# Optimization experiments

Measured on AMD Instinct MI355X. Metric: run time of the kernel, lower is better.

The kernel has to match this reference:

```python
import jax, jax.numpy as jnp
import numpy as np

N_NODES = 10000
N_EDGES = 160000
F_DIM = 64
H = 4


def setup_inputs() -> dict:
    key = jax.random.key(0)
    ks = jax.random.split(key, 10)
    s = 1.0 / np.sqrt(F_DIM)  # xavier-ish scale
    return {
        "x": jax.random.normal(ks[0], (N_NODES, F_DIM), jnp.float32),
        "edge_index": jax.random.randint(ks[1], (2, N_EDGES), 0, N_NODES),
        "edge_vec": jax.random.normal(ks[2], (N_EDGES, 3), jnp.float32),
        "edge_len": jax.random.uniform(ks[3], (N_EDGES,), jnp.float32, 0.1, 5.0),
        "w_proj_W": jax.random.normal(ks[4], (H, F_DIM, F_DIM), jnp.float32) * s,
        "radial_W": jax.random.normal(ks[5], (H, F_DIM, F_DIM), jnp.float32) * s,
        "tangential_W": jax.random.normal(ks[6], (H, F_DIM, F_DIM), jnp.float32) * s,
        "radial_score": jax.random.normal(ks[7], (H, F_DIM), jnp.float32) * s,
        "tangential_score": jax.random.normal(ks[8], (H, F_DIM), jnp.float32) * s,
        "radial_distance_log_scale": jnp.zeros((), jnp.float32),
        "radial_temp_bias": jnp.zeros((H,), jnp.float32),
        "radial_temp_weight": jnp.zeros((H,), jnp.float32),
        "w_out_W": jax.random.normal(ks[9], (F_DIM, F_DIM), jnp.float32) * s,
    }


def _segment_softmax(logits, receiver, num_nodes):
    # logits: [E, H]; softmax over all edges sharing the same receiver.
    # Equivalent to the original's degree-bucketed per-group softmax.
    m = jax.ops.segment_max(logits, receiver, num_segments=num_nodes)  # [N, H]
    a = jnp.exp(logits - m[receiver])
    d = jax.ops.segment_sum(a, receiver, num_segments=num_nodes)       # [N, H]
    return a / d[receiver]


def reference(x, edge_index, edge_vec, edge_len, w_proj_W, radial_W, tangential_W,
              radial_score, tangential_score, radial_distance_log_scale,
              radial_temp_bias, radial_temp_weight, w_out_W):
    sender, receiver = edge_index[0], edge_index[1]
    n = x.shape[0]

    # Per-head bias-free linear projections (o3.Linear on scalar irreps).
    energy = jnp.einsum('nf,hfg->hng', x, w_proj_W)       # [H, N, F]
    radial = jnp.einsum('nf,hfg->hng', x, radial_W)       # [H, N, F]
    tang = jnp.einsum('nf,hfg->hng', x, tangential_W)     # [H, N, F]

    e_d = energy[:, sender] - energy[:, receiver]                       # [H, E, F]
    r_d = jnp.transpose(radial[:, sender] - radial[:, receiver], (1, 0, 2))  # [E, H, F]
    t_d = jnp.transpose(tang[:, sender] - tang[:, receiver], (1, 0, 2))      # [E, H, F]

    scale = jax.nn.softplus(radial_distance_log_scale)
    r_log = jnp.einsum('hef,hf->eh', e_d, radial_score) - scale * edge_len[:, None]  # [E, H]
    temp = jax.nn.softplus(radial_temp_bias[None, :] + radial_temp_weight[None, :] * edge_len[:, None])
    r_log = r_log / (temp + 0.0001)
    t_log = jnp.einsum('hef,hf->eh', e_d, tangential_score)                          # [E, H]

    r_alpha = _segment_softmax(r_log, receiver, n)  # [E, H]
    t_alpha = _segment_softmax(t_log, receiver, n)  # [E, H]

    r_msg = jax.ops.segment_sum(r_alpha[:, :, None] * r_d, receiver, num_segments=n)  # [N, H, F]
    t_msg = jax.ops.segment_sum(t_alpha[:, :, None] * t_d, receiver, num_segments=n)  # [N, H, F]

    out = jnp.nan_to_num((r_msg + t_msg).mean(axis=1))  # mean over heads -> [N, F]
    return x + out @ w_out_W
```

## Files before the change

### kernel.cpp

```cpp
#include <hip/hip_runtime.h>
#include <math.h>

#define N_NODES 10000
#define N_EDGES 160000
#define CAP 64

typedef short bf16x8 __attribute__((ext_vector_type(8)));
typedef float f32x4 __attribute__((ext_vector_type(4)));

__device__ __forceinline__ float bf2f(unsigned short u) {
    return __uint_as_float(((unsigned int)u) << 16);
}
__device__ __forceinline__ unsigned short f2bf(float f) {
    unsigned int x = __float_as_uint(f);
    unsigned int r = (x + 0x7fffu + ((x >> 16) & 1u)) >> 16;
    return (unsigned short)r;
}
__device__ __forceinline__ float softplus_f(float x) {
    return fmaxf(x, 0.f) + log1pf(expf(-fabsf(x)));
}

#define NB_PROJ 628
#define NB_SCORE 40
#define NB_BUCKET 625

__global__ void __launch_bounds__(256) k_prep(const float* __restrict__ x,
                                              const float* __restrict__ wrad,
                                              const float* __restrict__ wtan,
                                              const float* __restrict__ wproj,
                                              const float* __restrict__ rsc,
                                              const float* __restrict__ tsc,
                                              const int* __restrict__ ei,
                                              const float* __restrict__ el,
                                              unsigned short* __restrict__ radb,
                                              unsigned short* __restrict__ tanb,
                                              float* __restrict__ rs,
                                              float* __restrict__ ts,
                                              int* __restrict__ cur,
                                              int2* __restrict__ sbuf) {
    __shared__ __align__(16) char smem[2 * 64 * 72 * 2];
    int b = blockIdx.x;
    int t = threadIdx.x;

    if (b < NB_PROJ) {
        unsigned short* wt0 = (unsigned short*)smem;
        unsigned short* wt1 = wt0 + 64 * 72;
        int h = b & 3;
        int nb = (b >> 2) * 64;
        const float* wr = wrad + h * 4096;
        const float* wtp = wtan + h * 4096;
        for (int i = 0; i < 16; ++i) {
            int e = t + 256 * i;
            int f = e >> 6, g = e & 63;
            wt0[g * 72 + f] = f2bf(wr[e]);
            wt1[g * 72 + f] = f2bf(wtp[e]);
        }
        __syncthreads();

        int wid = t >> 6, lane = t & 63;
        int q = lane >> 4, l16 = lane & 15;
        int node = nb + wid * 16 + l16;
        int nrow = min(node, N_NODES - 1);

        bf16x8 bfr[2];
#pragma unroll
        for (int kc = 0; kc < 2; ++kc) {
            const float* xp = x + nrow * 64 + kc * 32 + q * 8;
            float4 v0 = ((const float4*)xp)[0];
            float4 v1 = ((const float4*)xp)[1];
            bf16x8 bv;
            bv[0] = (short)f2bf(v0.x); bv[1] = (short)f2bf(v0.y);
            bv[2] = (short)f2bf(v0.z); bv[3] = (short)f2bf(v0.w);
            bv[4] = (short)f2bf(v1.x); bv[5] = (short)f2bf(v1.y);
            bv[6] = (short)f2bf(v1.z); bv[7] = (short)f2bf(v1.w);
            bfr[kc] = bv;
        }
#pragma unroll
        for (int gt = 0; gt < 4; ++gt) {
            f32x4 accr = {0.f, 0.f, 0.f, 0.f};
            f32x4 acct = {0.f, 0.f, 0.f, 0.f};
            int arow = gt * 16 + l16;
#pragma unroll
            for (int kc = 0; kc < 2; ++kc) {
                bf16x8 ar = *(const bf16x8*)&wt0[arow * 72 + kc * 32 + q * 8];
                bf16x8 at = *(const bf16x8*)&wt1[arow * 72 + kc * 32 + q * 8];
                accr = __builtin_amdgcn_mfma_f32_16x16x32_bf16(ar, bfr[kc], accr, 0, 0, 0);
                acct = __builtin_amdgcn_mfma_f32_16x16x32_bf16(at, bfr[kc], acct, 0, 0, 0);
            }
            if (node < N_NODES) {
                int g = gt * 16 + q * 4;
                ushort4 rv = make_ushort4(f2bf(accr[0]), f2bf(accr[1]),
                                          f2bf(accr[2]), f2bf(accr[3]));
                ushort4 tv = make_ushort4(f2bf(acct[0]), f2bf(acct[1]),
                                          f2bf(acct[2]), f2bf(acct[3]));
                *(ushort4*)(radb + node * 256 + h * 64 + g) = rv;
                *(ushort4*)(tanb + node * 256 + h * 64 + g) = tv;
            }
        }
    } else if (b < NB_PROJ + NB_SCORE) {
        float* vrl = (float*)smem;
        float* vtl = vrl + 256;
        {
            int h = t >> 6, f = t & 63;
            const float* wrow = wproj + h * 4096 + f * 64;
            const float* rsp = rsc + h * 64;
            const float* tsp = tsc + h * 64;
            float ar = 0.f, at = 0.f;
            for (int g = 0; g < 64; ++g) {
                float w = wrow[g];
                ar += w * rsp[g];
                at += w * tsp[g];
            }
            vrl[t] = ar;
            vtl[t] = at;
        }
        __syncthreads();
        int n = (b - NB_PROJ) * 256 + t;
        if (n >= N_NODES) return;
        const float4* xr = (const float4*)(x + n * 64);
        float accr[4] = {0.f, 0.f, 0.f, 0.f};
        float acct[4] = {0.f, 0.f, 0.f, 0.f};
        for (int i = 0; i < 16; ++i) {
            float4 xv = xr[i];
#pragma unroll
            for (int h = 0; h < 4; ++h) {
                float4 a = ((const float4*)vrl)[h * 16 + i];
                accr[h] += xv.x * a.x + xv.y * a.y + xv.z * a.z + xv.w * a.w;
                float4 bb = ((const float4*)vtl)[h * 16 + i];
                acct[h] += xv.x * bb.x + xv.y * bb.y + xv.z * bb.z + xv.w * bb.w;
            }
        }
        ((float4*)rs)[n] = make_float4(accr[0], accr[1], accr[2], accr[3]);
        ((float4*)ts)[n] = make_float4(acct[0], acct[1], acct[2], acct[3]);
    } else {
        int e = (b - NB_PROJ - NB_SCORE) * 256 + t;
        if (e >= N_EDGES) return;
        int s = ei[e];
        int r = ei[N_EDGES + e];
        float len = el[e];
        int pos = atomicAdd(&cur[r], 1);
        if (pos < CAP) sbuf[r * CAP + pos] = make_int2(s, __float_as_int(len));
    }
}

__global__ void __launch_bounds__(256) k_node(const int* __restrict__ cur,
                                              const int2* __restrict__ sbuf,
                                              const float* __restrict__ rs,
                                              const float* __restrict__ ts,
                                              const unsigned short* __restrict__ radb,
                                              const unsigned short* __restrict__ tanb,
                                              const float* __restrict__ rdls,
                                              const float* __restrict__ tb,
                                              const float* __restrict__ tw,
                                              const float* __restrict__ x,
                                              const float* __restrict__ wout,
                                              float* __restrict__ out) {
    __shared__ float wl[4096];
    __shared__ float alds[4][CAP][8];
    __shared__ int   slds[4][CAP];
    __shared__ float prelds[4][64];
    int t = threadIdx.x;
    for (int i = 0; i < 16; ++i) wl[t + 256 * i] = wout[t + 256 * i];

    int wid = t >> 6, lane = t & 63;
    int n = blockIdx.x * 4 + wid;
    int deg = min(cur[n], CAP);

    float4 rsr = ((const float4*)rs)[n];
    float4 tsr = ((const float4*)ts)[n];
    float scale = softplus_f(rdls[0]);
    float tb0 = tb[0], tb1 = tb[1], tb2 = tb[2], tb3 = tb[3];
    float tw0 = tw[0], tw1 = tw[1], tw2 = tw[2], tw3 = tw[3];

    const float NEG = -3.402823466e38f;
    float rl0 = NEG, rl1 = NEG, rl2 = NEG, rl3 = NEG;
    float tl0 = NEG, tl1 = NEG, tl2 = NEG, tl3 = NEG;
    int s_e = 0;
    if (lane < deg) {
        int2 sl = sbuf[n * CAP + lane];
        s_e = sl.x;
        float len = __int_as_float(sl.y);
        float4 rss = ((const float4*)rs)[s_e];
        float4 tss = ((const float4*)ts)[s_e];
        float sl0 = scale * len;
        float i0 = 1.f / (softplus_f(tb0 + tw0 * len) + 1e-4f);
        float i1 = 1.f / (softplus_f(tb1 + tw1 * len) + 1e-4f);
        float i2 = 1.f / (softplus_f(tb2 + tw2 * len) + 1e-4f);
        float i3 = 1.f / (softplus_f(tb3 + tw3 * len) + 1e-4f);
        rl0 = ((rss.x - rsr.x) - sl0) * i0;
        rl1 = ((rss.y - rsr.y) - sl0) * i1;
        rl2 = ((rss.z - rsr.z) - sl0) * i2;
        rl3 = ((rss.w - rsr.w) - sl0) * i3;
        tl0 = tss.x - tsr.x;
        tl1 = tss.y - tsr.y;
        tl2 = tss.z - tsr.z;
        tl3 = tss.w - tsr.w;
    }
    float mr0 = rl0, mr1 = rl1, mr2 = rl2, mr3 = rl3;
    float mt0 = tl0, mt1 = tl1, mt2 = tl2, mt3 = tl3;
#pragma unroll
    for (int d = 32; d >= 1; d >>= 1) {
        mr0 = fmaxf(mr0, __shfl_xor(mr0, d)); mr1 = fmaxf(mr1, __shfl_xor(mr1, d));
        mr2 = fmaxf(mr2, __shfl_xor(mr2, d)); mr3 = fmaxf(mr3, __shfl_xor(mr3, d));
        mt0 = fmaxf(mt0, __shfl_xor(mt0, d)); mt1 = fmaxf(mt1, __shfl_xor(mt1, d));
        mt2 = fmaxf(mt2, __shfl_xor(mt2, d)); mt3 = fmaxf(mt3, __shfl_xor(mt3, d));
    }
    float er0 = 0.f, er1 = 0.f, er2 = 0.f, er3 = 0.f;
    float et0 = 0.f, et1 = 0.f, et2 = 0.f, et3 = 0.f;
    if (lane < deg) {
        er0 = expf(rl0 - mr0); er1 = expf(rl1 - mr1);
        er2 = expf(rl2 - mr2); er3 = expf(rl3 - mr3);
        et0 = expf(tl0 - mt0); et1 = expf(tl1 - mt1);
        et2 = expf(tl2 - mt2); et3 = expf(tl3 - mt3);
    }
    float sr0 = er0, sr1 = er1, sr2 = er2, sr3 = er3;
    float st0 = et0, st1 = et1, st2 = et2, st3 = et3;
#pragma unroll
    for (int d = 32; d >= 1; d >>= 1) {
        sr0 += __shfl_xor(sr0, d); sr1 += __shfl_xor(sr1, d);
        sr2 += __shfl_xor(sr2, d); sr3 += __shfl_xor(sr3, d);
        st0 += __shfl_xor(st0, d); st1 += __shfl_xor(st1, d);
        st2 += __shfl_xor(st2, d); st3 += __shfl_xor(st3, d);
    }
    if (lane < deg) {
        float* ap = &alds[wid][lane][0];
        ((float4*)ap)[0] = make_float4(er0 / sr0, er1 / sr1, er2 / sr2, er3 / sr3);
        ((float4*)ap)[1] = make_float4(et0 / st0, et1 / st1, et2 / st2, et3 / st3);
        slds[wid][lane] = s_e;
    }

    int h = lane >> 4;
    int hb = h * 64 + ((lane & 15) << 2);
    float a0 = 0.f, a1 = 0.f, a2 = 0.f, a3 = 0.f;
    float b0 = 0.f, b1 = 0.f, b2 = 0.f, b3 = 0.f;
    int i = 0;
    for (; i + 2 <= deg; i += 2) {
        int s0 = slds[wid][i], s1 = slds[wid][i + 1];
        float ar0 = alds[wid][i][h],     at0 = alds[wid][i][4 + h];
        float ar1 = alds[wid][i + 1][h], at1 = alds[wid][i + 1][4 + h];
        ushort4 rv0 = *(const ushort4*)(radb + s0 * 256 + hb);
        ushort4 tv0 = *(const ushort4*)(tanb + s0 * 256 + hb);
        ushort4 rv1 = *(const ushort4*)(radb + s1 * 256 + hb);
        ushort4 tv1 = *(const ushort4*)(tanb + s1 * 256 + hb);
        a0 += ar0 * bf2f(rv0.x) + ar1 * bf2f(rv1.x);
        a1 += ar0 * bf2f(rv0.y) + ar1 * bf2f(rv1.y);
        a2 += ar0 * bf2f(rv0.z) + ar1 * bf2f(rv1.z);
        a3 += ar0 * bf2f(rv0.w) + ar1 * bf2f(rv1.w);
        b0 += at0 * bf2f(tv0.x) + at1 * bf2f(tv1.x);
        b1 += at0 * bf2f(tv0.y) + at1 * bf2f(tv1.y);
        b2 += at0 * bf2f(tv0.z) + at1 * bf2f(tv1.z);
        b3 += at0 * bf2f(tv0.w) + at1 * bf2f(tv1.w);
    }
    if (i < deg) {
        int s0 = slds[wid][i];
        float ar0 = alds[wid][i][h], at0 = alds[wid][i][4 + h];
        ushort4 rv0 = *(const ushort4*)(radb + s0 * 256 + hb);
        ushort4 tv0 = *(const ushort4*)(tanb + s0 * 256 + hb);
        a0 += ar0 * bf2f(rv0.x); a1 += ar0 * bf2f(rv0.y);
        a2 += ar0 * bf2f(rv0.z); a3 += ar0 * bf2f(rv0.w);
        b0 += at0 * bf2f(tv0.x); b1 += at0 * bf2f(tv0.y);
        b2 += at0 * bf2f(tv0.z); b3 += at0 * bf2f(tv0.w);
    }
    if (deg > 0) {
        ushort4 rv = *(const ushort4*)(radb + n * 256 + hb);
        ushort4 tv = *(const ushort4*)(tanb + n * 256 + hb);
        a0 -= bf2f(rv.x); a1 -= bf2f(rv.y); a2 -= bf2f(rv.z); a3 -= bf2f(rv.w);
        b0 -= bf2f(tv.x); b1 -= bf2f(tv.y); b2 -= bf2f(tv.z); b3 -= bf2f(tv.w);
    }
    float c0 = a0 + b0, c1 = a1 + b1, c2 = a2 + b2, c3 = a3 + b3;
    c0 += __shfl_xor(c0, 16); c0 += __shfl_xor(c0, 32);
    c1 += __shfl_xor(c1, 16); c1 += __shfl_xor(c1, 32);
    c2 += __shfl_xor(c2, 16); c2 += __shfl_xor(c2, 32);
    c3 += __shfl_xor(c3, 16); c3 += __shfl_xor(c3, 32);
    if (lane < 16) {
        ((float4*)&prelds[wid][0])[lane] =
            make_float4(c0 * 0.25f, c1 * 0.25f, c2 * 0.25f, c3 * 0.25f);
    }
    __syncthreads();

    float acc = 0.f;
    const float* pw = &prelds[wid][0];
#pragma unroll 4
    for (int gc = 0; gc < 16; ++gc) {
        float4 pv = ((const float4*)pw)[gc];
        acc += pv.x * wl[(4 * gc + 0) * 64 + lane];
        acc += pv.y * wl[(4 * gc + 1) * 64 + lane];
        acc += pv.z * wl[(4 * gc + 2) * 64 + lane];
        acc += pv.w * wl[(4 * gc + 3) * 64 + lane];
    }
    out[n * 64 + lane] = x[n * 64 + lane] + acc;
}

extern "C" void kernel_launch(void* const* d_in, const int* in_sizes, int n_in,
                              void* d_out, int out_size, void* d_ws, size_t ws_size,
                              hipStream_t stream) {
    const float* x     = (const float*)d_in[0];
    const int*   ei    = (const int*)d_in[1];
    const float* el    = (const float*)d_in[3];
    const float* wproj = (const float*)d_in[4];
    const float* wrad  = (const float*)d_in[5];
    const float* wtan  = (const float*)d_in[6];
    const float* rsc   = (const float*)d_in[7];
    const float* tsc   = (const float*)d_in[8];
    const float* rdls  = (const float*)d_in[9];
    const float* tb    = (const float*)d_in[10];
    const float* tw    = (const float*)d_in[11];
    const float* wout  = (const float*)d_in[12];
    float* out = (float*)d_out;

    char* w = (char*)d_ws;
    size_t o = 0;
    auto nxt = [&](size_t bytes) -> char* {
        char* p = w + o;
        o += (bytes + 255) & ~(size_t)255;
        return p;
    };
    unsigned short* radb = (unsigned short*)nxt((size_t)N_NODES * 256 * 2);
    unsigned short* tanb = (unsigned short*)nxt((size_t)N_NODES * 256 * 2);
    float* rs = (float*)nxt((size_t)N_NODES * 4 * 4);
    float* ts = (float*)nxt((size_t)N_NODES * 4 * 4);
    int*   cur = (int*)nxt((size_t)N_NODES * 4);
    int2*  sbuf = (int2*)nxt((size_t)N_NODES * CAP * 8);

    hipMemsetAsync(cur, 0, (size_t)N_NODES * 4, stream);

    k_prep<<<NB_PROJ + NB_SCORE + NB_BUCKET, 256, 0, stream>>>(
        x, wrad, wtan, wproj, rsc, tsc, ei, el, radb, tanb, rs, ts, cur, sbuf);
    k_node<<<2500, 256, 0, stream>>>(cur, sbuf, rs, ts, radb, tanb,
                                     rdls, tb, tw, x, wout, out);
}
```

Baseline: 132.9 us.

## Aggregate raw x per head then apply pre-multiplied projection·Wout via MFMA

The per-node radial and tangential projections are no longer precomputed. Each node instead accumulates attention-weighted raw sender x rows per head, and the receiver-term subtraction is handled by the same contraction. Combined weight matrices (per-head W·Wout, plus the negated sum for the self term, with the 1/4 head mean folded in) are built in the prep kernel. A 16-node block then does a 576-deep bf16 MFMA against them. This removes the 628 projection blocks and the bf16 radb/tanb gather traffic, but puts more FMA work into aggregation and a larger GEMM per block.

```diff
diff --git a/kernel.cpp b/kernel.cpp
--- a/kernel.cpp
+++ b/kernel.cpp
@@ -4,6 +4,11 @@
 #define N_NODES 10000
 #define N_EDGES 160000
 #define CAP 64
+
+#define NB_SCORE 40
+#define NB_BUCKET 625
+#define NB_WPP 9
+#define NB_D1 (NB_SCORE + NB_BUCKET + NB_WPP)
 
 typedef short bf16x8 __attribute__((ext_vector_type(8)));
 typedef float f32x4 __attribute__((ext_vector_type(4)));
@@ -20,86 +25,27 @@
     return fmaxf(x, 0.f) + log1pf(expf(-fabsf(x)));
 }
 
-#define NB_PROJ 628
-#define NB_SCORE 40
-#define NB_BUCKET 625
-
 __global__ void __launch_bounds__(256) k_prep(const float* __restrict__ x,
+                                              const float* __restrict__ wproj,
                                               const float* __restrict__ wrad,
                                               const float* __restrict__ wtan,
-                                              const float* __restrict__ wproj,
                                               const float* __restrict__ rsc,
                                               const float* __restrict__ tsc,
+                                              const float* __restrict__ wout,
                                               const int* __restrict__ ei,
                                               const float* __restrict__ el,
-                                              unsigned short* __restrict__ radb,
-                                              unsigned short* __restrict__ tanb,
                                               float* __restrict__ rs,
                                               float* __restrict__ ts,
                                               int* __restrict__ cur,
-                                              int2* __restrict__ sbuf) {
-    __shared__ __align__(16) char smem[2 * 64 * 72 * 2];
+                                              int2* __restrict__ sbuf,
+                                              unsigned short* __restrict__ wppT) {
+    __shared__ __align__(16) float smem[8192];
     int b = blockIdx.x;
     int t = threadIdx.x;
 
-    if (b < NB_PROJ) {
-        unsigned short* wt0 = (unsigned short*)smem;
-        unsigned short* wt1 = wt0 + 64 * 72;
-        int h = b & 3;
-        int nb = (b >> 2) * 64;
-        const float* wr = wrad + h * 4096;
-        const float* wtp = wtan + h * 4096;
-        for (int i = 0; i < 16; ++i) {
-            int e = t + 256 * i;
-            int f = e >> 6, g = e & 63;
-            wt0[g * 72 + f] = f2bf(wr[e]);
-            wt1[g * 72 + f] = f2bf(wtp[e]);
-        }
-        __syncthreads();
-
-        int wid = t >> 6, lane = t & 63;
-        int q = lane >> 4, l16 = lane & 15;
-        int node = nb + wid * 16 + l16;
-        int nrow = min(node, N_NODES - 1);
-
-        bf16x8 bfr[2];
-#pragma unroll
-        for (int kc = 0; kc < 2; ++kc) {
-            const float* xp = x + nrow * 64 + kc * 32 + q * 8;
-            float4 v0 = ((const float4*)xp)[0];
-            float4 v1 = ((const float4*)xp)[1];
-            bf16x8 bv;
-            bv[0] = (short)f2bf(v0.x); bv[1] = (short)f2bf(v0.y);
-            bv[2] = (short)f2bf(v0.z); bv[3] = (short)f2bf(v0.w);
-            bv[4] = (short)f2bf(v1.x); bv[5] = (short)f2bf(v1.y);
-            bv[6] = (short)f2bf(v1.z); bv[7] = (short)f2bf(v1.w);
-            bfr[kc] = bv;
-        }
-#pragma unroll
-        for (int gt = 0; gt < 4; ++gt) {
-            f32x4 accr = {0.f, 0.f, 0.f, 0.f};
-            f32x4 acct = {0.f, 0.f, 0.f, 0.f};
-            int arow = gt * 16 + l16;
-#pragma unroll
-            for (int kc = 0; kc < 2; ++kc) {
-                bf16x8 ar = *(const bf16x8*)&wt0[arow * 72 + kc * 32 + q * 8];
-                bf16x8 at = *(const bf16x8*)&wt1[arow * 72 + kc * 32 + q * 8];
-                accr = __builtin_amdgcn_mfma_f32_16x16x32_bf16(ar, bfr[kc], accr, 0, 0, 0);
-                acct = __builtin_amdgcn_mfma_f32_16x16x32_bf16(at, bfr[kc], acct, 0, 0, 0);
-            }
-            if (node < N_NODES) {
-                int g = gt * 16 + q * 4;
-                ushort4 rv = make_ushort4(f2bf(accr[0]), f2bf(accr[1]),
-                                          f2bf(accr[2]), f2bf(accr[3]));
-                ushort4 tv = make_ushort4(f2bf(acct[0]), f2bf(acct[1]),
-                                          f2bf(acct[2]), f2bf(acct[3]));
-                *(ushort4*)(radb + node * 256 + h * 64 + g) = rv;
-                *(ushort4*)(tanb + node * 256 + h * 64 + g) = tv;
-            }
-        }
-    } else if (b < NB_PROJ + NB_SCORE) {
-        float* vrl = (float*)smem;
-        float* vtl = vrl + 256;
+    if (b < NB_SCORE) {
+        float* vrl = smem;
+        float* vtl = smem + 256;
         {
             int h = t >> 6, f = t & 63;
             const float* wrow = wproj + h * 4096 + f * 64;
@@ -115,7 +61,7 @@
             vtl[t] = at;
         }
         __syncthreads();
-        int n = (b - NB_PROJ) * 256 + t;
+        int n = b * 256 + t;
         if (n >= N_NODES) return;
         const float4* xr = (const float4*)(x + n * 64);
         float accr[4] = {0.f, 0.f, 0.f, 0.f};
@@ -132,14 +78,40 @@
         }
         ((float4*)rs)[n] = make_float4(accr[0], accr[1], accr[2], accr[3]);
         ((float4*)ts)[n] = make_float4(acct[0], acct[1], acct[2], acct[3]);
-    } else {
-        int e = (b - NB_PROJ - NB_SCORE) * 256 + t;
+    } else if (b < NB_SCORE + NB_BUCKET) {
+        int e = (b - NB_SCORE) * 256 + t;
         if (e >= N_EDGES) return;
         int s = ei[e];
         int r = ei[N_EDGES + e];
         float len = el[e];
         int pos = atomicAdd(&cur[r], 1);
         if (pos < CAP) sbuf[r * CAP + pos] = make_int2(s, __float_as_int(len));
+    } else {
+        int k = b - NB_SCORE - NB_BUCKET;
+        float* wo = smem;
+        float* am = smem + 4096;
+        for (int i = 0; i < 16; ++i) wo[t + 256 * i] = wout[t + 256 * i];
+        if (k < 8) {
+            const float* M = (k < 4) ? (wrad + k * 4096) : (wtan + (k - 4) * 4096);
+            for (int i = 0; i < 16; ++i) am[t + 256 * i] = M[t + 256 * i];
+        } else {
+            for (int i = 0; i < 16; ++i) {
+                int e = t + 256 * i;
+                float s = 0.f;
+#pragma unroll
+                for (int h = 0; h < 4; ++h) s += wrad[h * 4096 + e] + wtan[h * 4096 + e];
+                am[e] = -s;
+            }
+        }
+        __syncthreads();
+        int c = t & 63;
+        int fg = t >> 6;
+        for (int j = 0; j < 16; ++j) {
+            int f = fg * 16 + j;
+            float acc = 0.f;
+            for (int g = 0; g < 64; ++g) acc += am[f * 64 + g] * wo[g * 64 + c];
+            wppT[c * 576 + k * 64 + f] = f2bf(acc * 0.25f);
+        }
     }
 }
 
@@ -147,148 +119,149 @@
                                               const int2* __restrict__ sbuf,
                                               const float* __restrict__ rs,
                                               const float* __restrict__ ts,
-                                              const unsigned short* __restrict__ radb,
-                                              const unsigned short* __restrict__ tanb,
                                               const float* __restrict__ rdls,
                                               const float* __restrict__ tb,
                                               const float* __restrict__ tw,
                                               const float* __restrict__ x,
-                                              const float* __restrict__ wout,
+                                              const unsigned short* __restrict__ wppT,
                                               float* __restrict__ out) {
-    __shared__ float wl[4096];
-    __shared__ float alds[4][CAP][8];
-    __shared__ int   slds[4][CAP];
-    __shared__ float prelds[4][64];
+    __shared__ __align__(16) unsigned short accL[16 * 584];
+    __shared__ __align__(16) float aldsb[4][CAP * 8];
+    __shared__ int sldsb[4][CAP];
     int t = threadIdx.x;
-    for (int i = 0; i < 16; ++i) wl[t + 256 * i] = wout[t + 256 * i];
-
     int wid = t >> 6, lane = t & 63;
-    int n = blockIdx.x * 4 + wid;
-    int deg = min(cur[n], CAP);
-
-    float4 rsr = ((const float4*)rs)[n];
-    float4 tsr = ((const float4*)ts)[n];
+    int blk = blockIdx.x;
+
     float scale = softplus_f(rdls[0]);
     float tb0 = tb[0], tb1 = tb[1], tb2 = tb[2], tb3 = tb[3];
     float tw0 = tw[0], tw1 = tw[1], tw2 = tw[2], tw3 = tw[3];
-
-    const float NEG = -3.402823466e38f;
-    float rl0 = NEG, rl1 = NEG, rl2 = NEG, rl3 = NEG;
-    float tl0 = NEG, tl1 = NEG, tl2 = NEG, tl3 = NEG;
-    int s_e = 0;
-    if (lane < deg) {
-        int2 sl = sbuf[n * CAP + lane];
-        s_e = sl.x;
-        float len = __int_as_float(sl.y);
-        float4 rss = ((const float4*)rs)[s_e];
-        float4 tss = ((const float4*)ts)[s_e];
-        float sl0 = scale * len;
-        float i0 = 1.f / (softplus_f(tb0 + tw0 * len) + 1e-4f);
-        float i1 = 1.f / (softplus_f(tb1 + tw1 * len) + 1e-4f);
-        float i2 = 1.f / (softplus_f(tb2 + tw2 * len) + 1e-4f);
-        float i3 = 1.f / (softplus_f(tb3 + tw3 * len) + 1e-4f);
-        rl0 = ((rss.x - rsr.x) - sl0) * i0;
-        rl1 = ((rss.y - rsr.y) - sl0) * i1;
-        rl2 = ((rss.z - rsr.z) - sl0) * i2;
-        rl3 = ((rss.w - rsr.w) - sl0) * i3;
-        tl0 = tss.x - tsr.x;
-        tl1 = tss.y - tsr.y;
-        tl2 = tss.z - tsr.z;
-        tl3 = tss.w - tsr.w;
-    }
-    float mr0 = rl0, mr1 = rl1, mr2 = rl2, mr3 = rl3;
-    float mt0 = tl0, mt1 = tl1, mt2 = tl2, mt3 = tl3;
-#pragma unroll
-    for (int d = 32; d >= 1; d >>= 1) {
-        mr0 = fmaxf(mr0, __shfl_xor(mr0, d)); mr1 = fmaxf(mr1, __shfl_xor(mr1, d));
-        mr2 = fmaxf(mr2, __shfl_xor(mr2, d)); mr3 = fmaxf(mr3, __shfl_xor(mr3, d));
-        mt0 = fmaxf(mt0, __shfl_xor(mt0, d)); mt1 = fmaxf(mt1, __shfl_xor(mt1, d));
-        mt2 = fmaxf(mt2, __shfl_xor(mt2, d)); mt3 = fmaxf(mt3, __shfl_xor(mt3, d));
-    }
-    float er0 = 0.f, er1 = 0.f, er2 = 0.f, er3 = 0.f;
-    float et0 = 0.f, et1 = 0.f, et2 = 0.f, et3 = 0.f;
-    if (lane < deg) {
-        er0 = expf(rl0 - mr0); er1 = expf(rl1 - mr1);
-        er2 = expf(rl2 - mr2); er3 = expf(rl3 - mr3);
-        et0 = expf(tl0 - mt0); et1 = expf(tl1 - mt1);
-        et2 = expf(tl2 - mt2); et3 = expf(tl3 - mt3);
-    }
-    float sr0 = er0, sr1 = er1, sr2 = er2, sr3 = er3;
-    float st0 = et0, st1 = et1, st2 = et2, st3 = et3;
-#pragma unroll
-    for (int d = 32; d >= 1; d >>= 1) {
-        sr0 += __shfl_xor(sr0, d); sr1 += __shfl_xor(sr1, d);
-        sr2 += __shfl_xor(sr2, d); sr3 += __shfl_xor(sr3, d);
-        st0 += __shfl_xor(st0, d); st1 += __shfl_xor(st1, d);
-        st2 += __shfl_xor(st2, d); st3 += __shfl_xor(st3, d);
-    }
-    if (lane < deg) {
-        float* ap = &alds[wid][lane][0];
-        ((float4*)ap)[0] = make_float4(er0 / sr0, er1 / sr1, er2 / sr2, er3 / sr3);
-        ((float4*)ap)[1] = make_float4(et0 / st0, et1 / st1, et2 / st2, et3 / st3);
-        slds[wid][lane] = s_e;
-    }
-
-    int h = lane >> 4;
-    int hb = h * 64 + ((lane & 15) << 2);
-    float a0 = 0.f, a1 = 0.f, a2 = 0.f, a3 = 0.f;
-    float b0 = 0.f, b1 = 0.f, b2 = 0.f, b3 = 0.f;
-    int i = 0;
-    for (; i + 2 <= deg; i += 2) {
-        int s0 = slds[wid][i], s1 = slds[wid][i + 1];
-        float ar0 = alds[wid][i][h],     at0 = alds[wid][i][4 + h];
-        float ar1 = alds[wid][i + 1][h], at1 = alds[wid][i + 1][4 + h];
-        ushort4 rv0 = *(const ushort4*)(radb + s0 * 256 + hb);
-        ushort4 tv0 = *(const ushort4*)(tanb + s0 * 256 + hb);
-        ushort4 rv1 = *(const ushort4*)(radb + s1 * 256 + hb);
-        ushort4 tv1 = *(const ushort4*)(tanb + s1 * 256 + hb);
-        a0 += ar0 * bf2f(rv0.x) + ar1 * bf2f(rv1.x);
-        a1 += ar0 * bf2f(rv0.y) + ar1 * bf2f(rv1.y);
-        a2 += ar0 * bf2f(rv0.z) + ar1 * bf2f(rv1.z);
-        a3 += ar0 * bf2f(rv0.w) + ar1 * bf2f(rv1.w);
-        b0 += at0 * bf2f(tv0.x) + at1 * bf2f(tv1.x);
-        b1 += at0 * bf2f(tv0.y) + at1 * bf2f(tv1.y);
-        b2 += at0 * bf2f(tv0.z) + at1 * bf2f(tv1.z);
-        b3 += at0 * bf2f(tv0.w) + at1 * bf2f(tv1.w);
-    }
-    if (i < deg) {
-        int s0 = slds[wid][i];
-        float ar0 = alds[wid][i][h], at0 = alds[wid][i][4 + h];
-        ushort4 rv0 = *(const ushort4*)(radb + s0 * 256 + hb);
-        ushort4 tv0 = *(const ushort4*)(tanb + s0 * 256 + hb);
-        a0 += ar0 * bf2f(rv0.x); a1 += ar0 * bf2f(rv0.y);
-        a2 += ar0 * bf2f(rv0.z); a3 += ar0 * bf2f(rv0.w);
-        b0 += at0 * bf2f(tv0.x); b1 += at0 * bf2f(tv0.y);
-        b2 += at0 * bf2f(tv0.z); b3 += at0 * bf2f(tv0.w);
-    }
-    if (deg > 0) {
-        ushort4 rv = *(const ushort4*)(radb + n * 256 + hb);
-        ushort4 tv = *(const ushort4*)(tanb + n * 256 + hb);
-        a0 -= bf2f(rv.x); a1 -= bf2f(rv.y); a2 -= bf2f(rv.z); a3 -= bf2f(rv.w);
-        b0 -= bf2f(tv.x); b1 -= bf2f(tv.y); b2 -= bf2f(tv.z); b3 -= bf2f(tv.w);
-    }
-    float c0 = a0 + b0, c1 = a1 + b1, c2 = a2 + b2, c3 = a3 + b3;
-    c0 += __shfl_xor(c0, 16); c0 += __shfl_xor(c0, 32);
-    c1 += __shfl_xor(c1, 16); c1 += __shfl_xor(c1, 32);
-    c2 += __shfl_xor(c2, 16); c2 += __shfl_xor(c2, 32);
-    c3 += __shfl_xor(c3, 16); c3 += __shfl_xor(c3, 32);
-    if (lane < 16) {
-        ((float4*)&prelds[wid][0])[lane] =
-            make_float4(c0 * 0.25f, c1 * 0.25f, c2 * 0.25f, c3 * 0.25f);
+    float* alds = aldsb[wid];
+    int*   slds = sldsb[wid];
+
+    for (int j = 0; j < 4; ++j) {
+        int n = blk * 16 + wid * 4 + j;
+        int row = wid * 4 + j;
+        int deg = min(cur[n], CAP);
+
+        float4 rsr = ((const float4*)rs)[n];
+        float4 tsr = ((const float4*)ts)[n];
+
+        const float NEG = -3.402823466e38f;
+        float rl0 = NEG, rl1 = NEG, rl2 = NEG, rl3 = NEG;
+        float tl0 = NEG, tl1 = NEG, tl2 = NEG, tl3 = NEG;
+        int s_e = 0;
+        if (lane < deg) {
+            int2 sl = sbuf[n * CAP + lane];
+            s_e = sl.x;
+            float len = __int_as_float(sl.y);
+            float4 rss = ((const float4*)rs)[s_e];
+            float4 tss = ((const float4*)ts)[s_e];
+            float sl0 = scale * len;
+            float i0 = 1.f / (softplus_f(tb0 + tw0 * len) + 1e-4f);
+            float i1 = 1.f / (softplus_f(tb1 + tw1 * len) + 1e-4f);
+            float i2 = 1.f / (softplus_f(tb2 + tw2 * len) + 1e-4f);
+            float i3 = 1.f / (softplus_f(tb3 + tw3 * len) + 1e-4f);
+            rl0 = ((rss.x - rsr.x) - sl0) * i0;
+            rl1 = ((rss.y - rsr.y) - sl0) * i1;
+            rl2 = ((rss.z - rsr.z) - sl0) * i2;
+            rl3 = ((rss.w - rsr.w) - sl0) * i3;
+            tl0 = tss.x - tsr.x;
+            tl1 = tss.y - tsr.y;
+            tl2 = tss.z - tsr.z;
+            tl3 = tss.w - tsr.w;
+        }
+        float mr0 = rl0, mr1 = rl1, mr2 = rl2, mr3 = rl3;
+        float mt0 = tl0, mt1 = tl1, mt2 = tl2, mt3 = tl3;
+#pragma unroll
+        for (int d = 32; d >= 1; d >>= 1) {
+            mr0 = fmaxf(mr0, __shfl_xor(mr0, d)); mr1 = fmaxf(mr1, __shfl_xor(mr1, d));
+            mr2 = fmaxf(mr2, __shfl_xor(mr2, d)); mr3 = fmaxf(mr3, __shfl_xor(mr3, d));
+            mt0 = fmaxf(mt0, __shfl_xor(mt0, d)); mt1 = fmaxf(mt1, __shfl_xor(mt1, d));
+            mt2 = fmaxf(mt2, __shfl_xor(mt2, d)); mt3 = fmaxf(mt3, __shfl_xor(mt3, d));
+        }
+        float er0 = 0.f, er1 = 0.f, er2 = 0.f, er3 = 0.f;
+        float et0 = 0.f, et1 = 0.f, et2 = 0.f, et3 = 0.f;
+        if (lane < deg) {
+            er0 = expf(rl0 - mr0); er1 = expf(rl1 - mr1);
+            er2 = expf(rl2 - mr2); er3 = expf(rl3 - mr3);
+            et0 = expf(tl0 - mt0); et1 = expf(tl1 - mt1);
+            et2 = expf(tl2 - mt2); et3 = expf(tl3 - mt3);
+        }
+        float sr0 = er0, sr1 = er1, sr2 = er2, sr3 = er3;
+        float st0 = et0, st1 = et1, st2 = et2, st3 = et3;
+#pragma unroll
+        for (int d = 32; d >= 1; d >>= 1) {
+            sr0 += __shfl_xor(sr0, d); sr1 += __shfl_xor(sr1, d);
+            sr2 += __shfl_xor(sr2, d); sr3 += __shfl_xor(sr3, d);
+            st0 += __shfl_xor(st0, d); st1 += __shfl_xor(st1, d);
+            st2 += __shfl_xor(st2, d); st3 += __shfl_xor(st3, d);
+        }
+        if (lane < deg) {
+            float* ap = alds + lane * 8;
+            ((float4*)ap)[0] = make_float4(er0 / sr0, er1 / sr1, er2 / sr2, er3 / sr3);
+            ((float4*)ap)[1] = make_float4(et0 / st0, et1 / st1, et2 / st2, et3 / st3);
+            slds[lane] = s_e;
+        }
+
+        float a0 = 0.f, a1 = 0.f, a2 = 0.f, a3 = 0.f;
+        float b0 = 0.f, b1 = 0.f, b2 = 0.f, b3 = 0.f;
+        int i = 0;
+        for (; i + 2 <= deg; i += 2) {
+            int s0 = slds[i], s1 = slds[i + 1];
+            float4 ar0 = ((const float4*)(alds + i * 8))[0];
+            float4 at0 = ((const float4*)(alds + i * 8))[1];
+            float4 ar1 = ((const float4*)(alds + (i + 1) * 8))[0];
+            float4 at1 = ((const float4*)(alds + (i + 1) * 8))[1];
+            float xv0 = x[s0 * 64 + lane];
+            float xv1 = x[s1 * 64 + lane];
+            a0 += ar0.x * xv0 + ar1.x * xv1;
+            a1 += ar0.y * xv0 + ar1.y * xv1;
+            a2 += ar0.z * xv0 + ar1.z * xv1;
+            a3 += ar0.w * xv0 + ar1.w * xv1;
+            b0 += at0.x * xv0 + at1.x * xv1;
+            b1 += at0.y * xv0 + at1.y * xv1;
+            b2 += at0.z * xv0 + at1.z * xv1;
+            b3 += at0.w * xv0 + at1.w * xv1;
+        }
+        if (i < deg) {
+            int s0 = slds[i];
+            float4 ar0 = ((const float4*)(alds + i * 8))[0];
+            float4 at0 = ((const float4*)(alds + i * 8))[1];
+            float xv0 = x[s0 * 64 + lane];
+            a0 += ar0.x * xv0; a1 += ar0.y * xv0; a2 += ar0.z * xv0; a3 += ar0.w * xv0;
+            b0 += at0.x * xv0; b1 += at0.y * xv0; b2 += at0.z * xv0; b3 += at0.w * xv0;
+        }
+        float c8 = (deg > 0) ? x[n * 64 + lane] : 0.f;
+
+        unsigned short* arow = accL + row * 584;
+        arow[0 * 64 + lane] = f2bf(a0);
+        arow[1 * 64 + lane] = f2bf(a1);
+        arow[2 * 64 + lane] = f2bf(a2);
+        arow[3 * 64 + lane] = f2bf(a3);
+        arow[4 * 64 + lane] = f2bf(b0);
+        arow[5 * 64 + lane] = f2bf(b1);
+        arow[6 * 64 + lane] = f2bf(b2);
+        arow[7 * 64 + lane] = f2bf(b3);
+        arow[8 * 64 + lane] = f2bf(c8);
     }
     __syncthreads();
 
-    float acc = 0.f;
-    const float* pw = &prelds[wid][0];
-#pragma unroll 4
-    for (int gc = 0; gc < 16; ++gc) {
-        float4 pv = ((const float4*)pw)[gc];
-        acc += pv.x * wl[(4 * gc + 0) * 64 + lane];
-        acc += pv.y * wl[(4 * gc + 1) * 64 + lane];
-        acc += pv.z * wl[(4 * gc + 2) * 64 + lane];
-        acc += pv.w * wl[(4 * gc + 3) * 64 + lane];
+    int c = lane & 15, q = lane >> 4;
+    f32x4 dacc = {0.f, 0.f, 0.f, 0.f};
+    const unsigned short* bp = wppT + (16 * wid + c) * 576 + q * 8;
+    const unsigned short* ap = accL + c * 584 + q * 8;
+#pragma unroll
+    for (int kc = 0; kc < 18; ++kc) {
+        bf16x8 af = *(const bf16x8*)(ap + kc * 32);
+        bf16x8 bf = *(const bf16x8*)(bp + kc * 32);
+        dacc = __builtin_amdgcn_mfma_f32_16x16x32_bf16(af, bf, dacc, 0, 0, 0);
     }
-    out[n * 64 + lane] = x[n * 64 + lane] + acc;
+#pragma unroll
+    for (int r = 0; r < 4; ++r) {
+        int node = blk * 16 + q * 4 + r;
+        int col = 16 * wid + c;
+        out[node * 64 + col] = x[node * 64 + col] + dacc[r];
+    }
 }
 
 extern "C" void kernel_launch(void* const* d_in, const int* in_sizes, int n_in,
@@ -315,17 +288,15 @@
         o += (bytes + 255) & ~(size_t)255;
         return p;
     };
-    unsigned short* radb = (unsigned short*)nxt((size_t)N_NODES * 256 * 2);
-    unsigned short* tanb = (unsigned short*)nxt((size_t)N_NODES * 256 * 2);
     float* rs = (float*)nxt((size_t)N_NODES * 4 * 4);
     float* ts = (float*)nxt((size_t)N_NODES * 4 * 4);
     int*   cur = (int*)nxt((size_t)N_NODES * 4);
     int2*  sbuf = (int2*)nxt((size_t)N_NODES * CAP * 8);
+    unsigned short* wppT = (unsigned short*)nxt((size_t)64 * 576 * 2);
 
     hipMemsetAsync(cur, 0, (size_t)N_NODES * 4, stream);
 
-    k_prep<<<NB_PROJ + NB_SCORE + NB_BUCKET, 256, 0, stream>>>(
-        x, wrad, wtan, wproj, rsc, tsc, ei, el, radb, tanb, rs, ts, cur, sbuf);
-    k_node<<<2500, 256, 0, stream>>>(cur, sbuf, rs, ts, radb, tanb,
-                                     rdls, tb, tw, x, wout, out);
-}
+    k_prep<<<NB_D1, 256, 0, stream>>>(x, wproj, wrad, wtan, rsc, tsc, wout,
+                                      ei, el, rs, ts, cur, sbuf, wppT);
+    k_node<<<625, 256, 0, stream>>>(cur, sbuf, rs, ts, rdls, tb, tw, x, wppT, out);
+}
```

New measurement: 137.5 us. 3.4% more time.
